# Performance work log

Hardware: AMD Instinct MI355X
Metric: run time of the kernel (lower is better)

Reference implementation:

```python
import jax, jax.numpy as jnp
import numpy as np

B, DIN, DOUT = 8192, 1024, 1024


def setup_inputs() -> dict:
    key = jax.random.key(0)
    ks = jax.random.split(key, 20)
    s = 0.02  # weight init scale to keep gate pre-activations sane
    inp = {
        "x": jax.random.normal(ks[0], (B, DIN), jnp.float32),
        "h": jax.random.normal(ks[1], (B, DOUT), jnp.float32),
        "c": jax.random.normal(ks[2], (B, DOUT), jnp.float32),
    }
    names = ["i", "f", "g", "o"]
    k = 3
    for n in names:
        inp[f"Wx{n}"] = jax.random.normal(ks[k], (DIN, DOUT), jnp.float32) * s; k += 1
        inp[f"Wh{n}"] = jax.random.normal(ks[k], (DOUT, DOUT), jnp.float32) * s; k += 1
        inp[f"bx{n}"] = jax.random.normal(ks[k], (DOUT,), jnp.float32) * s; k += 1
        inp[f"bh{n}"] = jax.random.normal(ks[k], (DOUT,), jnp.float32) * s; k += 1
    return inp


def reference(x, h, c,
              Wxi, Whi, bxi, bhi,
              Wxf, Whf, bxf, bhf,
              Wxg, Whg, bxg, bhg,
              Wxo, Who, bxo, bho):
    # Fuse the 8 separate Linear layers into 2 GEMMs on concatenated weights
    # (same math as summing per-gate x/h projections + both biases).
    Wx = jnp.concatenate([Wxi, Wxf, Wxg, Wxo], axis=1)   # [DIN, 4*DOUT]
    Wh = jnp.concatenate([Whi, Whf, Whg, Who], axis=1)   # [DOUT, 4*DOUT]
    b = jnp.concatenate([bxi + bhi, bxf + bhf, bxg + bhg, bxo + bho])  # [4*DOUT]
    z = x @ Wx + h @ Wh + b                               # [B, 4*DOUT]
    zi, zf, zg, zo = jnp.split(z, 4, axis=1)
    i = jax.nn.sigmoid(zi)
    f = jax.nn.sigmoid(zf)
    g = jnp.tanh(zg)
    o = jax.nn.sigmoid(zo)
    c_new = f * c + i * g
    h_new = o * jnp.tanh(c_new)
    return (h_new, c_new)
```

## Files before the change

### kernel.cpp

```cpp
#include <hip/hip_runtime.h>
#include <stdint.h>


typedef __attribute__((ext_vector_type(4))) int i32x4;
typedef __attribute__((ext_vector_type(8))) _Float16 half8;
typedef __attribute__((ext_vector_type(4))) _Float16 half4;
typedef __attribute__((ext_vector_type(4))) float f32x4;

__device__ __forceinline__ void gload_lds16(const void* g, void* l) {
  __builtin_amdgcn_global_load_lds(
      (const __attribute__((address_space(1))) void*)g,
      (__attribute__((address_space(3))) void*)l, 16, 0, 0);
}

__device__ __forceinline__ float sigf(float x) { return 1.0f / (1.0f + __expf(-x)); }
__device__ __forceinline__ float tanhf_(float x) { return 1.0f - 2.0f / (__expf(2.0f * x) + 1.0f); }
__device__ __forceinline__ int q8(float v, float s) {
  int q = (int)rintf(v * s);
  return q < -127 ? -127 : (q > 127 ? 127 : q);
}

#define FENCE asm volatile("" ::: "memory")
#define BAR do { FENCE; __builtin_amdgcn_s_barrier(); FENCE; } while (0)
#define LG0 do { asm volatile("s_waitcnt lgkmcnt(0)" ::: "memory"); \
                 __builtin_amdgcn_sched_barrier(0); } while (0)
#define VMC(n) asm volatile("s_waitcnt vmcnt(" #n ")" ::: "memory")

__global__ void lstm_scales(const float* __restrict__ x, const float* __restrict__ h,
                            const float* __restrict__ Wxi, const float* __restrict__ Whi,
                            const float* __restrict__ Wxf, const float* __restrict__ Whf,
                            const float* __restrict__ Wxg, const float* __restrict__ Whg,
                            const float* __restrict__ Wxo, const float* __restrict__ Who,
                            float* __restrict__ sxd, float* __restrict__ sxq,
                            float* __restrict__ swd, float* __restrict__ swq) {
  int b = blockIdx.x, t = threadIdx.x;
  if (b < 2048) {
    int row = b * 4 + (t >> 6), l = t & 63;
    const float* px = x + (size_t)row * 1024;
    const float* ph = h + (size_t)row * 1024;
    float m = 0.f;
    #pragma unroll
    for (int i = 0; i < 16; ++i) {
      m = fmaxf(m, fabsf(px[l + 64 * i]));
      m = fmaxf(m, fabsf(ph[l + 64 * i]));
    }
    #pragma unroll
    for (int off = 32; off; off >>= 1) m = fmaxf(m, __shfl_xor(m, off));
    if (l == 0) {
      m = fmaxf(m, 1e-12f);
      sxd[row] = m / 127.f;
      sxq[row] = 127.f / m;
    }
  } else {
    __shared__ float red[4][64];
    int np = (b - 2048) * 64 + (t & 63);
    int ks = t >> 6;
    int g = (np >> 4) & 3, j = ((np >> 6) << 4) | (np & 15);
    const float* Wx[4] = {Wxi, Wxf, Wxg, Wxo};
    const float* Wh[4] = {Whi, Whf, Whg, Who};
    const float* A = Wx[g];
    const float* Bm = Wh[g];
    float m = 0.f;
    for (int kk = 0; kk < 256; ++kk) {
      int k = ks * 256 + kk;
      m = fmaxf(m, fabsf(A[(size_t)k * 1024 + j]));
      m = fmaxf(m, fabsf(Bm[(size_t)k * 1024 + j]));
    }
    red[ks][t & 63] = m;
    __syncthreads();
    if (ks == 0) {
      m = fmaxf(fmaxf(red[0][t], red[1][t]), fmaxf(red[2][t], red[3][t]));
      m = fmaxf(m, 1e-12f);
      swd[np] = m / 127.f;
      swq[np] = 127.f / m;
    }
  }
}

__global__ void lstm_pack_i8(const float* __restrict__ x, const float* __restrict__ h,
                             const float* __restrict__ Wxi, const float* __restrict__ Whi,
                             const float* __restrict__ Wxf, const float* __restrict__ Whf,
                             const float* __restrict__ Wxg, const float* __restrict__ Whg,
                             const float* __restrict__ Wxo, const float* __restrict__ Who,
                             const float* __restrict__ bxi, const float* __restrict__ bhi,
                             const float* __restrict__ bxf, const float* __restrict__ bhf,
                             const float* __restrict__ bxg, const float* __restrict__ bhg,
                             const float* __restrict__ bxo, const float* __restrict__ bho,
                             const float* __restrict__ sxq, const float* __restrict__ swq,
                             signed char* __restrict__ Wt, signed char* __restrict__ Xh,
                             float* __restrict__ bias) {
  __shared__ float tile[32][33];
  int b = blockIdx.x, t = threadIdx.x;
  if (b < 8192) {
    int nt = b & 127, kt = b >> 7;
    int g = nt & 3, jt32 = nt >> 2;
    const float* Wx[4] = {Wxi, Wxf, Wxg, Wxo};
    const float* Wh[4] = {Whi, Whf, Whg, Who};
    int k0 = kt * 32;
    const float* src = (k0 < 1024) ? (Wx[g] + (size_t)k0 * 1024)
                                   : (Wh[g] + (size_t)(k0 - 1024) * 1024);
    int j0 = jt32 * 32;
    int cc = t & 31, r0 = t >> 5;
    #pragma unroll
    for (int p = 0; p < 4; ++p) {
      int r = p * 8 + r0;
      tile[r][cc] = src[(size_t)r * 1024 + j0 + cc];
    }
    __syncthreads();
    int jj = t >> 3, kk = (t & 7) * 4;
    int j = j0 + jj;
    int np = ((j >> 4) << 6) + g * 16 + (j & 15);
    float sq = swq[np];
    uint32_t w = 0;
    #pragma unroll
    for (int e = 0; e < 4; ++e) {
      int q = q8(tile[kk + e][jj], sq);
      w |= ((uint32_t)(q & 0xFF)) << (8 * e);
    }
    *(uint32_t*)(Wt + (size_t)np * 2048 + k0 + kk) = w;
  } else if (b < 16384) {
    int row = b - 8192;
    float sq = sxq[row];
    int k = t * 8;
    const float* src = (k < 1024) ? (x + (size_t)row * 1024 + k)
                                  : (h + (size_t)row * 1024 + (k - 1024));
    float4 f0 = *(const float4*)src;
    float4 f1 = *(const float4*)(src + 4);
    float v[8] = {f0.x, f0.y, f0.z, f0.w, f1.x, f1.y, f1.z, f1.w};
    uint64_t w = 0;
    #pragma unroll
    for (int e = 0; e < 8; ++e) {
      int q = q8(v[e], sq);
      w |= ((uint64_t)(uint32_t)(q & 0xFF)) << (8 * e);
    }
    *(uint64_t*)(Xh + (size_t)row * 2048 + k) = w;
  } else {
    int tt = (b - 16384) * 256 + t;
    if (tt < 4096) {
      const float* bx[4] = {bxi, bxf, bxg, bxo};
      const float* bh[4] = {bhi, bhf, bhg, bho};
      int q = tt >> 4, r = tt & 15;
      int g = q & 3, j = (q >> 2) * 16 + r;
      bias[tt] = bx[g][j] + bh[g][j];
    }
  }
}

__global__ __launch_bounds__(512, 2) void lstm_gemm_i8(
    const signed char* __restrict__ Xh, const signed char* __restrict__ Wt,
    const float* __restrict__ c, const float* __restrict__ bias,
    const float* __restrict__ sxd, const float* __restrict__ swd,
    float* __restrict__ out) {
  __shared__ signed char sA[2][256 * 64];
  __shared__ signed char sB[2][256 * 64];

  int bid = blockIdx.x;
  int xcd = bid & 7, idx = bid >> 3;
  int mt = (xcd >> 1) * 8 + (idx >> 3);
  int jt = (xcd & 1) * 8 + (idx & 7);
  int brow0 = mt * 256, bcol0 = jt * 256;

  int tid = threadIdx.x, lane = tid & 63, wave = tid >> 6;
  int wr = wave >> 2, wc = wave & 3;
  int l15 = lane & 15, l4 = lane >> 4;

  i32x4 acc[8][4] = {};

  int roff = (l4 ^ ((l15 >> 1) & 3)) * 16;
  int aoff0 = (wr * 128 + l15) * 64;
  int boff0 = (wc * 64 + l15) * 64;
  int ssl = ((tid & 3) ^ ((tid >> 3) & 3)) * 16;
  int srow = tid >> 2;

  auto stA = [&](int buf, int t, int a) {
    const signed char* src = Xh + (size_t)(brow0 + a * 128 + srow) * 2048 + t * 64 + ssl;
    gload_lds16(src, &sA[buf][(a * 128 + wave * 16) * 64]);
  };
  auto stB = [&](int buf, int t, int a) {
    const signed char* src = Wt + (size_t)(bcol0 + a * 128 + srow) * 2048 + t * 64 + ssl;
    gload_lds16(src, &sB[buf][(a * 128 + wave * 16) * 64]);
  };

#define STA(buf, t) do { stA(buf, t, 0); stA(buf, t, 1); } while (0)
#define STB(buf, t) do { stB(buf, t, 0); stB(buf, t, 1); } while (0)

#define LDBA(BUF) do { _Pragma("unroll") for (int nf = 0; nf < 4; ++nf) \
    bf[nf] = *(const i32x4*)&sB[BUF][boff0 + nf * 16 * 64 + roff]; } while (0)
#define LDAH(mh, BUF) do { _Pragma("unroll") for (int mi = 0; mi < 4; ++mi) \
    af[mi] = *(const i32x4*)&sA[BUF][aoff0 + ((mh) * 4 + mi) * 16 * 64 + roff]; } while (0)
#define MMH(mh) do {                                                          \
    __builtin_amdgcn_s_setprio(1);                                            \
    _Pragma("unroll") for (int mi = 0; mi < 4; ++mi)                          \
    _Pragma("unroll") for (int nf = 0; nf < 4; ++nf)                          \
      acc[(mh) * 4 + mi][nf] = __builtin_amdgcn_mfma_i32_16x16x64_i8(         \
          af[mi], bf[nf], acc[(mh) * 4 + mi][nf], 0, 0, 0);                   \
    __builtin_amdgcn_s_setprio(0); } while (0)

  STA(0, 0); STB(0, 0); STB(1, 1);
  VMC(2);
  BAR;

  i32x4 af[4], bf[4];

#pragma unroll 1
  for (int i = 0; i < 16; ++i) {
    const int u = 2 * i + 1, v = 2 * i + 2, w = 2 * i + 3;
    const bool pf = (i < 15);

    STA(1, u);
    LDBA(0); LDAH(0, 0);
    LG0; MMH(0);
    BAR;
    if (pf) STB(0, v);
    LDAH(1, 0);
    LG0; MMH(1);
    if (pf) { VMC(2); }
    else    { VMC(0); }
    BAR;
    if (pf) STA(0, v);
    LDBA(1); LDAH(0, 1);
    LG0; MMH(0);
    BAR;
    if (pf) STB(1, w);
    LDAH(1, 1);
    LG0; MMH(1);
    if (pf) { VMC(2); }
    BAR;
  }
#undef STA
#undef STB
#undef LDBA
#undef LDAH
#undef MMH

  int j = jt * 64 + wc * 16 + l15;
  int nbase = bcol0 + wc * 64 + l15;
  float sw0 = swd[nbase + 0];
  float sw1 = swd[nbase + 16];
  float sw2 = swd[nbase + 32];
  float sw3 = swd[nbase + 48];
  float bi  = bias[nbase + 0];
  float bff = bias[nbase + 16];
  float bg  = bias[nbase + 32];
  float bo  = bias[nbase + 48];
  float* hout = out;
  float* cout = out + (size_t)8192 * 1024;
  #pragma unroll
  for (int m = 0; m < 8; ++m) {
    #pragma unroll
    for (int r = 0; r < 4; ++r) {
      int grow = brow0 + wr * 128 + m * 16 + l4 * 4 + r;
      float sx = sxd[grow];
      size_t o = (size_t)grow * 1024 + j;
      float zi = (float)acc[m][0][r] * (sx * sw0) + bi;
      float zf = (float)acc[m][1][r] * (sx * sw1) + bff;
      float zg = (float)acc[m][2][r] * (sx * sw2) + bg;
      float zo = (float)acc[m][3][r] * (sx * sw3) + bo;
      float ig = sigf(zi);
      float fg = sigf(zf);
      float gg = tanhf_(zg);
      float og = sigf(zo);
      float cold = c[o];
      float cn = fg * cold + ig * gg;
      hout[o] = og * tanhf_(cn);
      cout[o] = cn;
    }
  }
}


__global__ void lstm_pack_w_v1(const float* __restrict__ Wxi, const float* __restrict__ Whi,
                               const float* __restrict__ Wxf, const float* __restrict__ Whf,
                               const float* __restrict__ Wxg, const float* __restrict__ Whg,
                               const float* __restrict__ Wxo, const float* __restrict__ Who,
                               _Float16* __restrict__ Wt) {
  __shared__ float tile[32][33];
  int nt = blockIdx.x;
  int kt = blockIdx.y;
  int g = nt & 3, jt = nt >> 2;
  const float* Wx[4] = {Wxi, Wxf, Wxg, Wxo};
  const float* Wh[4] = {Whi, Whf, Whg, Who};
  int k0 = kt * 32;
  const float* src = (k0 < 1024) ? (Wx[g] + (size_t)k0 * 1024)
                                 : (Wh[g] + (size_t)(k0 - 1024) * 1024);
  int j0 = jt * 32;
  int t = threadIdx.x;
  int cc = t & 31, r0 = t >> 5;
  #pragma unroll
  for (int p = 0; p < 4; ++p) {
    int r = p * 8 + r0;
    tile[r][cc] = src[(size_t)r * 1024 + j0 + cc];
  }
  __syncthreads();
  int jj = t >> 3, kk = (t & 7) * 4;
  half4 v;
  v[0] = (_Float16)tile[kk + 0][jj];
  v[1] = (_Float16)tile[kk + 1][jj];
  v[2] = (_Float16)tile[kk + 2][jj];
  v[3] = (_Float16)tile[kk + 3][jj];
  _Float16* dst = Wt + (size_t)(nt * 32 + jj) * 2048 + k0 + kk;
  *(half4*)dst = v;
}

__global__ void lstm_pack_bias_v1(const float* __restrict__ bxi, const float* __restrict__ bhi,
                                  const float* __restrict__ bxf, const float* __restrict__ bhf,
                                  const float* __restrict__ bxg, const float* __restrict__ bhg,
                                  const float* __restrict__ bxo, const float* __restrict__ bho,
                                  float* __restrict__ bias) {
  int t = blockIdx.x * 256 + threadIdx.x;
  if (t >= 4096) return;
  const float* bx[4] = {bxi, bxf, bxg, bxo};
  const float* bh[4] = {bhi, bhf, bhg, bho};
  int jt = t >> 7, g = (t >> 5) & 3, jj = t & 31;
  int j = jt * 32 + jj;
  bias[t] = bx[g][j] + bh[g][j];
}

__global__ __launch_bounds__(256, 2) void lstm_gemm_v1(
    const float* __restrict__ x, const float* __restrict__ h, const float* __restrict__ c,
    const _Float16* __restrict__ Wt, const float* __restrict__ bias,
    float* __restrict__ out) {
  __shared__ ushort sA[128 * 64];
  __shared__ ushort sB[128 * 64];
  int bid = blockIdx.x;
  int sbid = (bid & 7) * 256 + (bid >> 3);
  int mt = sbid >> 5, jt = sbid & 31;
  int brow0 = mt * 128;
  int tid = threadIdx.x;
  int lane = tid & 63, wave = tid >> 6;
  int wr = wave >> 1, wc = wave & 1;
  f32x4 acc[4][4] = {};
  int ar = tid >> 3;
  int as = tid & 7;
  int l3 = lane >> 3, l7w = lane & 7;
  int bsw = ((l7w ^ l3) << 3);
  int l15 = lane & 15, l4 = lane >> 4, l7 = lane & 7;
  for (int kt = 0; kt < 32; ++kt) {
    int k0 = kt * 64;
    const float* asrc = (k0 < 1024) ? (x + k0) : (h + (k0 - 1024));
    #pragma unroll
    for (int stp = 0; stp < 4; ++stp) {
      int row = stp * 32 + ar;
      const float* p = asrc + (size_t)(brow0 + row) * 1024 + as * 8;
      float4 f0 = *(const float4*)p;
      float4 f1 = *(const float4*)(p + 4);
      half8 hv;
      hv[0] = (_Float16)f0.x; hv[1] = (_Float16)f0.y;
      hv[2] = (_Float16)f0.z; hv[3] = (_Float16)f0.w;
      hv[4] = (_Float16)f1.x; hv[5] = (_Float16)f1.y;
      hv[6] = (_Float16)f1.z; hv[7] = (_Float16)f1.w;
      *(half8*)&sA[row * 64 + ((as ^ (row & 7)) << 3)] = hv;
    }
    #pragma unroll
    for (int ccall = 0; ccall < 4; ++ccall) {
      int rowbase = ccall * 32 + wave * 8;
      int grow = jt * 128 + rowbase + l3;
      const _Float16* src = Wt + (size_t)grow * 2048 + k0 + bsw;
      gload_lds16(src, &sB[rowbase * 64]);
    }
    __syncthreads();
    #pragma unroll
    for (int ks = 0; ks < 2; ++ks) {
      half8 af[4], bfr[4];
      #pragma unroll
      for (int mi = 0; mi < 4; ++mi) {
        int row = wr * 64 + mi * 16 + l15;
        af[mi] = *(const half8*)&sA[row * 64 + (((ks * 4 + l4) ^ l7) << 3)];
      }
      #pragma unroll
      for (int g = 0; g < 4; ++g) {
        int nr = g * 32 + wc * 16 + l15;
        bfr[g] = *(const half8*)&sB[nr * 64 + (((ks * 4 + l4) ^ l7) << 3)];
      }
      #pragma unroll
      for (int mi = 0; mi < 4; ++mi)
        #pragma unroll
        for (int g = 0; g < 4; ++g)
          acc[mi][g] = __builtin_amdgcn_mfma_f32_16x16x32_f16(af[mi], bfr[g], acc[mi][g], 0, 0, 0);
    }
    __syncthreads();
  }
  int j = jt * 32 + wc * 16 + l15;
  int nb = jt * 128 + wc * 16 + l15;
  float bi  = bias[nb + 0];
  float bff = bias[nb + 32];
  float bg  = bias[nb + 64];
  float bo  = bias[nb + 96];
  float* hout = out;
  float* cout = out + (size_t)8192 * 1024;
  #pragma unroll
  for (int mi = 0; mi < 4; ++mi) {
    #pragma unroll
    for (int r = 0; r < 4; ++r) {
      int grow = brow0 + wr * 64 + mi * 16 + l4 * 4 + r;
      size_t idx = (size_t)grow * 1024 + j;
      float zi = acc[mi][0][r] + bi;
      float zf = acc[mi][1][r] + bff;
      float zg = acc[mi][2][r] + bg;
      float zo = acc[mi][3][r] + bo;
      float ig = sigf(zi);
      float fg = sigf(zf);
      float gg = tanhf_(zg);
      float og = sigf(zo);
      float cold = c[idx];
      float cn = fg * cold + ig * gg;
      hout[idx] = og * tanhf_(cn);
      cout[idx] = cn;
    }
  }
}

extern "C" void kernel_launch(void* const* d_in, const int* in_sizes, int n_in,
                              void* d_out, int out_size, void* d_ws, size_t ws_size,
                              hipStream_t stream) {
  const float* x   = (const float*)d_in[0];
  const float* h   = (const float*)d_in[1];
  const float* c   = (const float*)d_in[2];
  const float* Wxi = (const float*)d_in[3];
  const float* Whi = (const float*)d_in[4];
  const float* bxi = (const float*)d_in[5];
  const float* bhi = (const float*)d_in[6];
  const float* Wxf = (const float*)d_in[7];
  const float* Whf = (const float*)d_in[8];
  const float* bxf = (const float*)d_in[9];
  const float* bhf = (const float*)d_in[10];
  const float* Wxg = (const float*)d_in[11];
  const float* Whg = (const float*)d_in[12];
  const float* bxg = (const float*)d_in[13];
  const float* bhg = (const float*)d_in[14];
  const float* Wxo = (const float*)d_in[15];
  const float* Who = (const float*)d_in[16];
  const float* bxo = (const float*)d_in[17];
  const float* bho = (const float*)d_in[18];
  float* out = (float*)d_out;

  const size_t WT_B  = (size_t)4096 * 2048;
  const size_t XH_B  = (size_t)8192 * 2048;
  const size_t NEED = WT_B + XH_B + 4096 * 4 + 8192 * 8 + 4096 * 8;

  if (ws_size >= NEED) {
    signed char* Wt = (signed char*)d_ws;
    signed char* Xh = (signed char*)d_ws + WT_B;
    char* p = (char*)d_ws + WT_B + XH_B;
    float* bias = (float*)p;             p += 4096 * 4;
    float* sxd  = (float*)p;             p += 8192 * 4;
    float* sxq  = (float*)p;             p += 8192 * 4;
    float* swd  = (float*)p;             p += 4096 * 4;
    float* swq  = (float*)p;
    lstm_scales<<<2112, 256, 0, stream>>>(x, h, Wxi, Whi, Wxf, Whf, Wxg, Whg,
                                          Wxo, Who, sxd, sxq, swd, swq);
    lstm_pack_i8<<<16400, 256, 0, stream>>>(x, h, Wxi, Whi, Wxf, Whf, Wxg, Whg,
                                            Wxo, Who, bxi, bhi, bxf, bhf,
                                            bxg, bhg, bxo, bho, sxq, swq,
                                            Wt, Xh, bias);
    lstm_gemm_i8<<<512, 512, 0, stream>>>(Xh, Wt, c, bias, sxd, swd, out);
  } else {
    _Float16* Wt = (_Float16*)d_ws;
    float* bias  = (float*)((char*)d_ws + (size_t)4096 * 2048 * 2);
    lstm_pack_w_v1<<<dim3(128, 64), 256, 0, stream>>>(Wxi, Whi, Wxf, Whf, Wxg, Whg, Wxo, Who, Wt);
    lstm_pack_bias_v1<<<16, 256, 0, stream>>>(bxi, bhi, bxf, bhf, bxg, bhg, bxo, bho, bias);
    lstm_gemm_v1<<<2048, 256, 0, stream>>>(x, h, c, Wt, bias, out);
  }
}
```

Measured before the change: 137.6 us.

## Fuse activation row-max into quantize pass and use coalesced atomic weight column max

Activation row scales are now computed inside the quantize kernel with a block reduction, so x and h are read once instead of twice. Weight column max moves to a separate kernel that reads row slabs coalesced and merges results with atomicMax on float bits. The max is taken from absolute values, so the bits order correctly as unsigned ints. This replaces the old strided column-walk scale kernel, at the cost of a memset and atomics, and the GEMM derives weight scales from colmax directly.

```diff
diff --git a/kernel.cpp b/kernel.cpp
--- a/kernel.cpp
+++ b/kernel.cpp
@@ -26,73 +26,82 @@
                  __builtin_amdgcn_sched_barrier(0); } while (0)
 #define VMC(n) asm volatile("s_waitcnt vmcnt(" #n ")" ::: "memory")
 
-__global__ void lstm_scales(const float* __restrict__ x, const float* __restrict__ h,
-                            const float* __restrict__ Wxi, const float* __restrict__ Whi,
-                            const float* __restrict__ Wxf, const float* __restrict__ Whf,
-                            const float* __restrict__ Wxg, const float* __restrict__ Whg,
-                            const float* __restrict__ Wxo, const float* __restrict__ Who,
-                            float* __restrict__ sxd, float* __restrict__ sxq,
-                            float* __restrict__ swd, float* __restrict__ swq) {
+__global__ void lstm_colmax(const float* __restrict__ Wxi, const float* __restrict__ Wxf,
+                            const float* __restrict__ Wxg, const float* __restrict__ Wxo,
+                            const float* __restrict__ Whi, const float* __restrict__ Whf,
+                            const float* __restrict__ Whg, const float* __restrict__ Who,
+                            unsigned int* __restrict__ colmax) {
+  __shared__ float cm[1024];
   int b = blockIdx.x, t = threadIdx.x;
-  if (b < 2048) {
-    int row = b * 4 + (t >> 6), l = t & 63;
-    const float* px = x + (size_t)row * 1024;
-    const float* ph = h + (size_t)row * 1024;
-    float m = 0.f;
-    #pragma unroll
-    for (int i = 0; i < 16; ++i) {
-      m = fmaxf(m, fabsf(px[l + 64 * i]));
-      m = fmaxf(m, fabsf(ph[l + 64 * i]));
-    }
-    #pragma unroll
-    for (int off = 32; off; off >>= 1) m = fmaxf(m, __shfl_xor(m, off));
-    if (l == 0) {
-      m = fmaxf(m, 1e-12f);
-      sxd[row] = m / 127.f;
-      sxq[row] = 127.f / m;
-    }
-  } else {
-    __shared__ float red[4][64];
-    int np = (b - 2048) * 64 + (t & 63);
-    int ks = t >> 6;
-    int g = (np >> 4) & 3, j = ((np >> 6) << 4) | (np & 15);
-    const float* Wx[4] = {Wxi, Wxf, Wxg, Wxo};
-    const float* Wh[4] = {Whi, Whf, Whg, Who};
-    const float* A = Wx[g];
-    const float* Bm = Wh[g];
-    float m = 0.f;
-    for (int kk = 0; kk < 256; ++kk) {
-      int k = ks * 256 + kk;
-      m = fmaxf(m, fabsf(A[(size_t)k * 1024 + j]));
-      m = fmaxf(m, fabsf(Bm[(size_t)k * 1024 + j]));
-    }
-    red[ks][t & 63] = m;
-    __syncthreads();
-    if (ks == 0) {
-      m = fmaxf(fmaxf(red[0][t], red[1][t]), fmaxf(red[2][t], red[3][t]));
-      m = fmaxf(m, 1e-12f);
-      swd[np] = m / 127.f;
-      swq[np] = 127.f / m;
-    }
-  }
-}
-
-__global__ void lstm_pack_i8(const float* __restrict__ x, const float* __restrict__ h,
-                             const float* __restrict__ Wxi, const float* __restrict__ Whi,
-                             const float* __restrict__ Wxf, const float* __restrict__ Whf,
-                             const float* __restrict__ Wxg, const float* __restrict__ Whg,
-                             const float* __restrict__ Wxo, const float* __restrict__ Who,
-                             const float* __restrict__ bxi, const float* __restrict__ bhi,
-                             const float* __restrict__ bxf, const float* __restrict__ bhf,
-                             const float* __restrict__ bxg, const float* __restrict__ bhg,
-                             const float* __restrict__ bxo, const float* __restrict__ bho,
-                             const float* __restrict__ sxq, const float* __restrict__ swq,
-                             signed char* __restrict__ Wt, signed char* __restrict__ Xh,
-                             float* __restrict__ bias) {
-  __shared__ float tile[32][33];
+  int m = b >> 6;
+  int r0 = (b & 63) * 16;
+  const float* Ws[8] = {Wxi, Wxf, Wxg, Wxo, Whi, Whf, Whg, Who};
+  const float* src = Ws[m] + (size_t)r0 * 1024;
+  #pragma unroll
+  for (int i = 0; i < 4; ++i) cm[t + 256 * i] = 0.f;
+  __syncthreads();
+  for (int r = 0; r < 16; ++r) {
+    #pragma unroll
+    for (int c4 = 0; c4 < 4; ++c4) {
+      int col = t + 256 * c4;
+      float v = fabsf(src[(size_t)r * 1024 + col]);
+      cm[col] = fmaxf(cm[col], v);
+    }
+  }
+  __syncthreads();
+  int g = m & 3;
+  #pragma unroll
+  for (int i = 0; i < 4; ++i) {
+    int j = t + 256 * i;
+    int np = ((j >> 4) << 6) + g * 16 + (j & 15);
+    atomicMax(&colmax[np], __float_as_uint(cm[j]));
+  }
+}
+
+__global__ void lstm_quant(const float* __restrict__ x, const float* __restrict__ h,
+                           const float* __restrict__ Wxi, const float* __restrict__ Whi,
+                           const float* __restrict__ Wxf, const float* __restrict__ Whf,
+                           const float* __restrict__ Wxg, const float* __restrict__ Whg,
+                           const float* __restrict__ Wxo, const float* __restrict__ Who,
+                           const float* __restrict__ bxi, const float* __restrict__ bhi,
+                           const float* __restrict__ bxf, const float* __restrict__ bhf,
+                           const float* __restrict__ bxg, const float* __restrict__ bhg,
+                           const float* __restrict__ bxo, const float* __restrict__ bho,
+                           const unsigned int* __restrict__ colmax,
+                           signed char* __restrict__ Wt, signed char* __restrict__ Xh,
+                           float* __restrict__ bias, float* __restrict__ sxd) {
   int b = blockIdx.x, t = threadIdx.x;
   if (b < 8192) {
-    int nt = b & 127, kt = b >> 7;
+    __shared__ float wm[4];
+    int row = b;
+    int k = t * 8;
+    const float* src = (k < 1024) ? (x + (size_t)row * 1024 + k)
+                                  : (h + (size_t)row * 1024 + (k - 1024));
+    float4 f0 = *(const float4*)src;
+    float4 f1 = *(const float4*)(src + 4);
+    float v[8] = {f0.x, f0.y, f0.z, f0.w, f1.x, f1.y, f1.z, f1.w};
+    float m = 0.f;
+    #pragma unroll
+    for (int e = 0; e < 8; ++e) m = fmaxf(m, fabsf(v[e]));
+    #pragma unroll
+    for (int off = 32; off; off >>= 1) m = fmaxf(m, __shfl_xor(m, off));
+    if ((t & 63) == 0) wm[t >> 6] = m;
+    __syncthreads();
+    m = fmaxf(fmaxf(wm[0], wm[1]), fmaxf(wm[2], wm[3]));
+    m = fmaxf(m, 1e-12f);
+    float sq = 127.f / m;
+    uint64_t w = 0;
+    #pragma unroll
+    for (int e = 0; e < 8; ++e) {
+      int q = q8(v[e], sq);
+      w |= ((uint64_t)(uint32_t)(q & 0xFF)) << (8 * e);
+    }
+    *(uint64_t*)(Xh + (size_t)row * 2048 + k) = w;
+    if (t == 0) sxd[row] = m * (1.f / 127.f);
+  } else if (b < 16384) {
+    __shared__ float tile[32][33];
+    int bb = b - 8192;
+    int nt = bb & 127, kt = bb >> 7;
     int g = nt & 3, jt32 = nt >> 2;
     const float* Wx[4] = {Wxi, Wxf, Wxg, Wxo};
     const float* Wh[4] = {Whi, Whf, Whg, Who};
@@ -110,7 +119,8 @@
     int jj = t >> 3, kk = (t & 7) * 4;
     int j = j0 + jj;
     int np = ((j >> 4) << 6) + g * 16 + (j & 15);
-    float sq = swq[np];
+    float mw = fmaxf(__uint_as_float(colmax[np]), 1e-12f);
+    float sq = 127.f / mw;
     uint32_t w = 0;
     #pragma unroll
     for (int e = 0; e < 4; ++e) {
@@ -118,22 +128,6 @@
       w |= ((uint32_t)(q & 0xFF)) << (8 * e);
     }
     *(uint32_t*)(Wt + (size_t)np * 2048 + k0 + kk) = w;
-  } else if (b < 16384) {
-    int row = b - 8192;
-    float sq = sxq[row];
-    int k = t * 8;
-    const float* src = (k < 1024) ? (x + (size_t)row * 1024 + k)
-                                  : (h + (size_t)row * 1024 + (k - 1024));
-    float4 f0 = *(const float4*)src;
-    float4 f1 = *(const float4*)(src + 4);
-    float v[8] = {f0.x, f0.y, f0.z, f0.w, f1.x, f1.y, f1.z, f1.w};
-    uint64_t w = 0;
-    #pragma unroll
-    for (int e = 0; e < 8; ++e) {
-      int q = q8(v[e], sq);
-      w |= ((uint64_t)(uint32_t)(q & 0xFF)) << (8 * e);
-    }
-    *(uint64_t*)(Xh + (size_t)row * 2048 + k) = w;
   } else {
     int tt = (b - 16384) * 256 + t;
     if (tt < 4096) {
@@ -149,7 +143,7 @@
 __global__ __launch_bounds__(512, 2) void lstm_gemm_i8(
     const signed char* __restrict__ Xh, const signed char* __restrict__ Wt,
     const float* __restrict__ c, const float* __restrict__ bias,
-    const float* __restrict__ sxd, const float* __restrict__ swd,
+    const float* __restrict__ sxd, const unsigned int* __restrict__ colmax,
     float* __restrict__ out) {
   __shared__ signed char sA[2][256 * 64];
   __shared__ signed char sB[2][256 * 64];
@@ -211,16 +205,19 @@
     LDBA(0); LDAH(0, 0);
     LG0; MMH(0);
     BAR;
+
     if (pf) STB(0, v);
     LDAH(1, 0);
     LG0; MMH(1);
     if (pf) { VMC(2); }
     else    { VMC(0); }
     BAR;
+
     if (pf) STA(0, v);
     LDBA(1); LDAH(0, 1);
     LG0; MMH(0);
     BAR;
+
     if (pf) STB(1, w);
     LDAH(1, 1);
     LG0; MMH(1);
@@ -235,10 +232,11 @@
 
   int j = jt * 64 + wc * 16 + l15;
   int nbase = bcol0 + wc * 64 + l15;
-  float sw0 = swd[nbase + 0];
-  float sw1 = swd[nbase + 16];
-  float sw2 = swd[nbase + 32];
-  float sw3 = swd[nbase + 48];
+  const float inv127 = 1.f / 127.f;
+  float sw0 = fmaxf(__uint_as_float(colmax[nbase + 0]),  1e-12f) * inv127;
+  float sw1 = fmaxf(__uint_as_float(colmax[nbase + 16]), 1e-12f) * inv127;
+  float sw2 = fmaxf(__uint_as_float(colmax[nbase + 32]), 1e-12f) * inv127;
+  float sw3 = fmaxf(__uint_as_float(colmax[nbase + 48]), 1e-12f) * inv127;
   float bi  = bias[nbase + 0];
   float bff = bias[nbase + 16];
   float bg  = bias[nbase + 32];
@@ -434,26 +432,24 @@
   const float* bho = (const float*)d_in[18];
   float* out = (float*)d_out;
 
-  const size_t WT_B  = (size_t)4096 * 2048;
-  const size_t XH_B  = (size_t)8192 * 2048;
-  const size_t NEED = WT_B + XH_B + 4096 * 4 + 8192 * 8 + 4096 * 8;
+  const size_t WT_B = (size_t)4096 * 2048;
+  const size_t XH_B = (size_t)8192 * 2048;
+  const size_t NEED = WT_B + XH_B + 4096 * 4 + 8192 * 4 + 4096 * 4;
 
   if (ws_size >= NEED) {
     signed char* Wt = (signed char*)d_ws;
     signed char* Xh = (signed char*)d_ws + WT_B;
     char* p = (char*)d_ws + WT_B + XH_B;
-    float* bias = (float*)p;             p += 4096 * 4;
-    float* sxd  = (float*)p;             p += 8192 * 4;
-    float* sxq  = (float*)p;             p += 8192 * 4;
-    float* swd  = (float*)p;             p += 4096 * 4;
-    float* swq  = (float*)p;
-    lstm_scales<<<2112, 256, 0, stream>>>(x, h, Wxi, Whi, Wxf, Whf, Wxg, Whg,
-                                          Wxo, Who, sxd, sxq, swd, swq);
-    lstm_pack_i8<<<16400, 256, 0, stream>>>(x, h, Wxi, Whi, Wxf, Whf, Wxg, Whg,
-                                            Wxo, Who, bxi, bhi, bxf, bhf,
-                                            bxg, bhg, bxo, bho, sxq, swq,
-                                            Wt, Xh, bias);
-    lstm_gemm_i8<<<512, 512, 0, stream>>>(Xh, Wt, c, bias, sxd, swd, out);
+    float* bias = (float*)p;               p += 4096 * 4;
+    float* sxd  = (float*)p;               p += 8192 * 4;
+    unsigned int* colmax = (unsigned int*)p;
+    hipMemsetAsync(colmax, 0, 4096 * 4, stream);
+    lstm_colmax<<<512, 256, 0, stream>>>(Wxi, Wxf, Wxg, Wxo, Whi, Whf, Whg, Who, colmax);
+    lstm_quant<<<16400, 256, 0, stream>>>(x, h, Wxi, Whi, Wxf, Whf, Wxg, Whg,
+                                          Wxo, Who, bxi, bhi, bxf, bhf,
+                                          bxg, bhg, bxo, bho, colmax,
+                                          Wt, Xh, bias, sxd);
+    lstm_gemm_i8<<<512, 512, 0, stream>>>(Xh, Wt, c, bias, sxd, colmax, out);
   } else {
     _Float16* Wt = (_Float16*)d_ws;
     float* bias  = (float*)((char*)d_ws + (size_t)4096 * 2048 * 2);
```

Result: no change. 135.6 us, median of 5 (-1.4%).
